# Kernel optimization log

Hardware: AMD Instinct MI355X
Metric: run time of the kernel (lower is better)

Reference implementation:

```python
import jax, jax.numpy as jnp
import numpy as np

B, C, N = 8, 512, 2048  # batch, channels (=size), tokens


def setup_inputs() -> dict:
    key = jax.random.key(0)
    ks = jax.random.split(key, 9)
    s = 1.0 / np.sqrt(C)
    return {
        "q": jax.random.normal(ks[0], (B, C, N), dtype=jnp.float32),
        "k": jax.random.normal(ks[1], (B, C, N), dtype=jnp.float32),
        "v": jax.random.normal(ks[2], (B, C, N), dtype=jnp.float32),
        "wq": jax.random.normal(ks[3], (C, C), dtype=jnp.float32) * s,
        "bq": jax.random.normal(ks[4], (C,), dtype=jnp.float32) * s,
        "wk": jax.random.normal(ks[5], (C, C), dtype=jnp.float32) * s,
        "bk": jax.random.normal(ks[6], (C,), dtype=jnp.float32) * s,
        "wv": jax.random.normal(ks[7], (C, C), dtype=jnp.float32) * s,
        "bv": jax.random.normal(ks[8], (C,), dtype=jnp.float32) * s,
    }


def _proj(x, w, b):
    # 1x1 conv over channels: out[b,c,n] = sum_i w[c,i] x[b,i,n] + b[c]
    return jnp.einsum('ci,bin->bcn', w, x) + b[None, :, None]


def reference(q, k, v, wq, bq, wk, bk, wv, bv):
    residual = q                                   # [B, C, N]
    qp = _proj(q, wq, bq).transpose(0, 2, 1)       # [B, N, C]
    kp = _proj(k, wk, bk).transpose(0, 2, 1)       # [B, N, C]
    vp = _proj(v, wv, bv).transpose(0, 2, 1)       # [B, N, C]
    attn = jnp.einsum('bnc,bmc->bnm', qp, kp)      # raw QK^T, no scale/softmax
    out = jnp.einsum('bnm,bmc->bnc', attn, vp)     # [B, N, C]
    return out.transpose(0, 2, 1) + residual       # [B, C, N]
```

## Files before the change

kernel.cpp:

```cpp
#include <hip/hip_runtime.h>
#include <hip/hip_bf16.h>
#include <stdint.h>

#define B_ 8
#define C_ 512
#define N_ 2048

typedef __bf16 bf16_t;
typedef bf16_t bf16x8 __attribute__((ext_vector_type(8)));
typedef bf16_t bf16x4 __attribute__((ext_vector_type(4)));
typedef float f32x4 __attribute__((ext_vector_type(4)));

__global__ __launch_bounds__(256) void prep_all_kernel(
    const float* __restrict__ q, const float* __restrict__ kin,
    const float* __restrict__ vin,
    const float* __restrict__ wq, const float* __restrict__ wk,
    const float* __restrict__ wv, const float* __restrict__ bq,
    const float* __restrict__ bk,
    bf16_t* __restrict__ qT, bf16_t* __restrict__ kc, bf16_t* __restrict__ vc,
    bf16_t* __restrict__ WqT, bf16_t* __restrict__ WkT, bf16_t* __restrict__ Wvb,
    float* __restrict__ s1p, float* __restrict__ sk, float* __restrict__ sv)
{
    __shared__ bf16_t tileA[64][65];
    __shared__ bf16_t tileB[64][65];
    __shared__ float red256[256];
    __shared__ float redr[4][4];
    const int bid = blockIdx.x;
    const int tid = threadIdx.x;

    if (bid < 1024) {
        const int b = bid >> 7;
        const int rem = bid & 127;
        const int c0 = (rem >> 4) * 64;
        const int n0 = (rem & 15) * 128;
        const float* src = q + (size_t)b * C_ * N_;
        bf16_t* dT = qT + (size_t)b * N_ * C_;
        const int cx = (tid & 15) * 4, ry = tid >> 4;
        float4 fa[4], fb[4];
#pragma unroll
        for (int p = 0; p < 4; ++p) {
            const int r = ry + p * 16;
            fa[p] = *(const float4*)&src[(size_t)(c0 + r) * N_ + n0 + cx];
            fb[p] = *(const float4*)&src[(size_t)(c0 + r) * N_ + n0 + 64 + cx];
        }
#pragma unroll
        for (int p = 0; p < 4; ++p) {
            const int r = ry + p * 16;
            tileA[r][cx + 0] = (bf16_t)fa[p].x; tileA[r][cx + 1] = (bf16_t)fa[p].y;
            tileA[r][cx + 2] = (bf16_t)fa[p].z; tileA[r][cx + 3] = (bf16_t)fa[p].w;
            tileB[r][cx + 0] = (bf16_t)fb[p].x; tileB[r][cx + 1] = (bf16_t)fb[p].y;
            tileB[r][cx + 2] = (bf16_t)fb[p].z; tileB[r][cx + 3] = (bf16_t)fb[p].w;
        }
        __syncthreads();
#pragma unroll
        for (int p = 0; p < 4; ++p) {
            const int r = ry + p * 16;
            bf16x4 o0, o1;
            o0[0] = tileA[cx + 0][r]; o0[1] = tileA[cx + 1][r];
            o0[2] = tileA[cx + 2][r]; o0[3] = tileA[cx + 3][r];
            *(bf16x4*)&dT[(size_t)(n0 + r) * C_ + c0 + cx] = o0;
            o1[0] = tileB[cx + 0][r]; o1[1] = tileB[cx + 1][r];
            o1[2] = tileB[cx + 2][r]; o1[3] = tileB[cx + 3][r];
            *(bf16x4*)&dT[(size_t)(n0 + 64 + r) * C_ + c0 + cx] = o1;
        }
    } else if (bid < 1217) {
        const int t = bid - 1024;
        if (t < 128) {
            const float* src = (t < 64) ? wq : wk;
            bf16_t* dst = (t < 64) ? WqT : WkT;
            const int j = t & 63;
            const int i0 = (j & 7) * 64, c0 = (j >> 3) * 64;
            const int cx = (tid & 15) * 4, ry = tid >> 4;
#pragma unroll
            for (int r = ry; r < 64; r += 16) {
                float4 f = *(const float4*)&src[(size_t)(c0 + r) * C_ + i0 + cx];
                tileA[r][cx + 0] = (bf16_t)f.x; tileA[r][cx + 1] = (bf16_t)f.y;
                tileA[r][cx + 2] = (bf16_t)f.z; tileA[r][cx + 3] = (bf16_t)f.w;
            }
            __syncthreads();
#pragma unroll
            for (int r = ry; r < 64; r += 16) {
                bf16x4 o;
                o[0] = tileA[cx + 0][r]; o[1] = tileA[cx + 1][r];
                o[2] = tileA[cx + 2][r]; o[3] = tileA[cx + 3][r];
                *(bf16x4*)&dst[(size_t)(i0 + r) * C_ + c0 + cx] = o;
            }
        } else if (t < 192) {
            const int j = t - 128;
#pragma unroll
            for (int p = 0; p < 4; ++p) {
                const int i = j * 4096 + p * 1024 + tid * 4;
                float4 f = *(const float4*)(wv + i);
                bf16x4 o;
                o[0] = (bf16_t)f.x; o[1] = (bf16_t)f.y;
                o[2] = (bf16_t)f.z; o[3] = (bf16_t)f.w;
                *(bf16x4*)(Wvb + i) = o;
            }
        } else {
            float p = bk[tid] * bq[tid] + bk[tid + 256] * bq[tid + 256];
            red256[tid] = p;
            __syncthreads();
            for (int s = 128; s > 0; s >>= 1) {
                if (tid < s) red256[tid] += red256[tid + s];
                __syncthreads();
            }
            if (tid == 0) s1p[0] = red256[0];
        }
    } else {
        const int r = bid - 1217;
        const int selv = r >> 10;
        const int row0 = (r & 1023) * 4;
        const float* src = (selv ? vin : kin) + (size_t)row0 * N_;
        bf16_t* dst = (selv ? vc : kc) + (size_t)row0 * N_;
        const int i = tid * 8;
        float4 f[4][2];
#pragma unroll
        for (int rr = 0; rr < 4; ++rr) {
            f[rr][0] = *(const float4*)(src + (size_t)rr * N_ + i);
            f[rr][1] = *(const float4*)(src + (size_t)rr * N_ + i + 4);
        }
        const int lane = tid & 63, wave = tid >> 6;
#pragma unroll
        for (int rr = 0; rr < 4; ++rr) {
            bf16x8 o;
            o[0] = (bf16_t)f[rr][0].x; o[1] = (bf16_t)f[rr][0].y;
            o[2] = (bf16_t)f[rr][0].z; o[3] = (bf16_t)f[rr][0].w;
            o[4] = (bf16_t)f[rr][1].x; o[5] = (bf16_t)f[rr][1].y;
            o[6] = (bf16_t)f[rr][1].z; o[7] = (bf16_t)f[rr][1].w;
            *(bf16x8*)(dst + (size_t)rr * N_ + i) = o;
            float s = f[rr][0].x + f[rr][0].y + f[rr][0].z + f[rr][0].w +
                      f[rr][1].x + f[rr][1].y + f[rr][1].z + f[rr][1].w;
#pragma unroll
            for (int d = 1; d < 64; d <<= 1) s += __shfl_xor(s, d, 64);
            if (lane == 0) redr[wave][rr] = s;
        }
        __syncthreads();
        if (tid < 4)
            (selv ? sv : sk)[row0 + tid] =
                redr[0][tid] + redr[1][tid] + redr[2][tid] + redr[3][tid];
    }
}

__global__ __launch_bounds__(256, 2) void dkv_M_kernel(
    const bf16_t* __restrict__ kc, const bf16_t* __restrict__ vc,
    bf16_t* __restrict__ Dp,
    const bf16_t* __restrict__ WqT, const bf16_t* __restrict__ WkT,
    bf16_t* __restrict__ M, const float* __restrict__ bq,
    const float* __restrict__ bk, float* __restrict__ gk,
    float* __restrict__ va)
{
    __shared__ __align__(16) bf16_t As[128 * 64];
    __shared__ __align__(16) bf16_t Bs[128 * 64];
    const int f = blockIdx.x;
    const int tid = threadIdx.x, lane = tid & 63, wave = tid >> 6;
    const int wr = wave >> 1, wc = wave & 1;
    const size_t sCC = (size_t)C_ * C_;
    const size_t sBN = (size_t)N_ * C_;

    if (f < 512) {
        const int zz = f >> 4;
        const int bz = zz >> 2, sp = zz & 3;
        const int t4 = f & 15;
        const int m0 = (t4 >> 2) * 128, n0 = (t4 & 3) * 128;
        const int kbeg = sp * 512;
        const bf16_t* Ab = kc + (size_t)bz * sBN;
        const bf16_t* Bb = vc + (size_t)bz * sBN;

        f32x4 acc[4][4];
#pragma unroll
        for (int i = 0; i < 4; ++i)
#pragma unroll
            for (int j = 0; j < 4; ++j) acc[i][j] = 0.f;

        const int srow = tid >> 3;
        const int scol = ((tid & 7) ^ (srow & 7)) * 8;
        const int ldso = tid * 16;

        for (int t = 0; t < 8; ++t) {
            const bf16_t* ga = Ab + (size_t)(m0 + srow) * N_ + kbeg + t * 64 + scol;
            const bf16_t* gb = Bb + (size_t)(n0 + srow) * N_ + kbeg + t * 64 + scol;
#pragma unroll
            for (int p = 0; p < 4; ++p)
                __builtin_amdgcn_global_load_lds(
                    (const __attribute__((address_space(1))) void*)(ga + (size_t)p * 32 * N_),
                    (__attribute__((address_space(3))) void*)((char*)As + ldso + p * 4096),
                    16, 0, 0);
#pragma unroll
            for (int p = 0; p < 4; ++p)
                __builtin_amdgcn_global_load_lds(
                    (const __attribute__((address_space(1))) void*)(gb + (size_t)p * 32 * N_),
                    (__attribute__((address_space(3))) void*)((char*)Bs + ldso + p * 4096),
                    16, 0, 0);
            __syncthreads();

#pragma unroll
            for (int kk = 0; kk < 64; kk += 32) {
                bf16x8 af[4], bfr[4];
                const int kcol = kk + (lane >> 4) * 8;
                const int kcn = kcol >> 3;
#pragma unroll
                for (int m = 0; m < 4; ++m) {
                    const int r = wr * 64 + (lane & 15) + m * 16;
                    af[m] = *(const bf16x8*)((const char*)As + r * 128 +
                                             ((kcn ^ (r & 7)) << 4));
                }
#pragma unroll
                for (int n = 0; n < 4; ++n) {
                    const int r = wc * 64 + (lane & 15) + n * 16;
                    bfr[n] = *(const bf16x8*)((const char*)Bs + r * 128 +
                                              ((kcn ^ (r & 7)) << 4));
                }
#pragma unroll
                for (int m = 0; m < 4; ++m)
#pragma unroll
                    for (int n = 0; n < 4; ++n)
                        acc[m][n] = __builtin_amdgcn_mfma_f32_16x16x32_bf16(
                            af[m], bfr[n], acc[m][n], 0, 0, 0);
            }
            __syncthreads();
        }

        const int rj = (lane >> 4) * 4;
        const int cc = lane & 15;
#pragma unroll
        for (int m = 0; m < 4; ++m)
#pragma unroll
            for (int n = 0; n < 4; ++n) {
                const int col = n0 + wc * 64 + n * 16 + cc;
                f32x4 vv = acc[m][n];
#pragma unroll
                for (int j = 0; j < 4; ++j) {
                    const int row = m0 + wr * 64 + m * 16 + rj + j;
                    Dp[(size_t)zz * sCC + (size_t)row * C_ + col] = (bf16_t)vv[j];
                }
            }
    } else if (f < 576) {
        const int g = f - 512;
        const int m0 = (g >> 3) * 64, n0 = (g & 7) * 64;
        f32x4 acc[2][2];
#pragma unroll
        for (int i = 0; i < 2; ++i)
#pragma unroll
            for (int j = 0; j < 2; ++j) acc[i][j] = 0.f;
        const int srow = tid >> 3;
        const int scol = ((tid & 7) ^ (srow & 7)) * 8;
        const int ldso = tid * 16;
        for (int t = 0; t < 8; ++t) {
            const bf16_t* ga = WqT + (size_t)(m0 + srow) * C_ + t * 64 + scol;
            const bf16_t* gb = WkT + (size_t)(n0 + srow) * C_ + t * 64 + scol;
#pragma unroll
            for (int p = 0; p < 2; ++p)
                __builtin_amdgcn_global_load_lds(
                    (const __attribute__((address_space(1))) void*)(ga + (size_t)p * 32 * C_),
                    (__attribute__((address_space(3))) void*)((char*)As + ldso + p * 4096),
                    16, 0, 0);
#pragma unroll
            for (int p = 0; p < 2; ++p)
                __builtin_amdgcn_global_load_lds(
                    (const __attribute__((address_space(1))) void*)(gb + (size_t)p * 32 * C_),
                    (__attribute__((address_space(3))) void*)((char*)Bs + ldso + p * 4096),
                    16, 0, 0);
            __syncthreads();
#pragma unroll
            for (int kk = 0; kk < 64; kk += 32) {
                bf16x8 af[2], bfr[2];
                const int kcol = kk + (lane >> 4) * 8;
                const int kcn = kcol >> 3;
#pragma unroll
                for (int m = 0; m < 2; ++m) {
                    const int r = wr * 32 + (lane & 15) + m * 16;
                    af[m] = *(const bf16x8*)((const char*)As + r * 128 +
                                             ((kcn ^ (r & 7)) << 4));
                }
#pragma unroll
                for (int n = 0; n < 2; ++n) {
                    const int r = wc * 32 + (lane & 15) + n * 16;
                    bfr[n] = *(const bf16x8*)((const char*)Bs + r * 128 +
                                              ((kcn ^ (r & 7)) << 4));
                }
#pragma unroll
                for (int m = 0; m < 2; ++m)
#pragma unroll
                    for (int n = 0; n < 2; ++n)
                        acc[m][n] = __builtin_amdgcn_mfma_f32_16x16x32_bf16(
                            af[m], bfr[n], acc[m][n], 0, 0, 0);
            }
            __syncthreads();
        }
        const int rj = (lane >> 4) * 4;
        const int cc = lane & 15;
#pragma unroll
        for (int m = 0; m < 2; ++m)
#pragma unroll
            for (int n = 0; n < 2; ++n) {
                const int col = n0 + wc * 32 + n * 16 + cc;
                f32x4 vv = acc[m][n];
#pragma unroll
                for (int j = 0; j < 4; ++j) {
                    const int row = m0 + wr * 32 + m * 16 + rj + j;
                    M[(size_t)row * C_ + col] = (bf16_t)vv[j];
                }
            }
    } else {
        const int j = f - 576;
        const bf16_t* W = (j < 8) ? WkT : WqT;
        const float* bb = (j < 8) ? bq : bk;
        float* out = (j < 8) ? gk : va;
        const int row = (j & 7) * 64 + (tid >> 2);
        const int c0 = (tid & 3) * 128;
        const bf16_t* rp = W + (size_t)row * C_ + c0;
        float acc = 0.f;
#pragma unroll
        for (int e = 0; e < 128; e += 8) {
            bf16x8 vv = *(const bf16x8*)(rp + e);
#pragma unroll
            for (int x = 0; x < 8; ++x) acc += (float)vv[x] * bb[c0 + e + x];
        }
        acc += __shfl_xor(acc, 1, 64);
        acc += __shfl_xor(acc, 2, 64);
        if ((tid & 3) == 0) out[row] = acc;
    }
}

__global__ __launch_bounds__(256) void p1_fused_kernel(
    const bf16_t* __restrict__ Wvb, const bf16_t* __restrict__ Dp,
    bf16_t* __restrict__ P1, const bf16_t* __restrict__ M,
    const float* __restrict__ sk, const float* __restrict__ sv,
    const float* __restrict__ gk, const float* __restrict__ s1p,
    float* __restrict__ u, float* __restrict__ vbraw, float* __restrict__ s2)
{
    __shared__ __align__(16) bf16_t As[64 * 64];
    __shared__ __align__(16) bf16_t Bs[64 * 64];
    __shared__ float svec[C_];
    __shared__ float red[256];
    const int f = blockIdx.x;
    const int tid = threadIdx.x, lane = tid & 63, wave = tid >> 6;
    const int wr = wave >> 1, wc = wave & 1;
    const size_t sCC = (size_t)C_ * C_;

    if (f < 512) {
        const int bz = f >> 6;
        const int m0 = ((f >> 3) & 7) * 64, n0 = (f & 7) * 64;
        f32x4 acc[2][2];
#pragma unroll
        for (int i = 0; i < 2; ++i)
#pragma unroll
            for (int j = 0; j < 2; ++j) acc[i][j] = 0.f;
        const int srow = tid >> 3;
        const int scol = ((tid & 7) ^ (srow & 7)) * 8;
        const int ldso = tid * 16;

        for (int sp = 0; sp < 4; ++sp) {
            const bf16_t* Bb = Dp + (size_t)(bz * 4 + sp) * sCC;
            for (int t = 0; t < 8; ++t) {
                const bf16_t* ga = Wvb + (size_t)(m0 + srow) * C_ + t * 64 + scol;
                const bf16_t* gb = Bb + (size_t)(n0 + srow) * C_ + t * 64 + scol;
#pragma unroll
                for (int p = 0; p < 2; ++p)
                    __builtin_amdgcn_global_load_lds(
                        (const __attribute__((address_space(1))) void*)(ga + (size_t)p * 32 * C_),
                        (__attribute__((address_space(3))) void*)((char*)As + ldso + p * 4096),
                        16, 0, 0);
#pragma unroll
                for (int p = 0; p < 2; ++p)
                    __builtin_amdgcn_global_load_lds(
                        (const __attribute__((address_space(1))) void*)(gb + (size_t)p * 32 * C_),
                        (__attribute__((address_space(3))) void*)((char*)Bs + ldso + p * 4096),
                        16, 0, 0);
                __syncthreads();
#pragma unroll
                for (int kk = 0; kk < 64; kk += 32) {
                    bf16x8 af[2], bfr[2];
                    const int kcol = kk + (lane >> 4) * 8;
                    const int kcn = kcol >> 3;
#pragma unroll
                    for (int m = 0; m < 2; ++m) {
                        const int r = wr * 32 + (lane & 15) + m * 16;
                        af[m] = *(const bf16x8*)((const char*)As + r * 128 +
                                                 ((kcn ^ (r & 7)) << 4));
                    }
#pragma unroll
                    for (int n = 0; n < 2; ++n) {
                        const int r = wc * 32 + (lane & 15) + n * 16;
                        bfr[n] = *(const bf16x8*)((const char*)Bs + r * 128 +
                                                  ((kcn ^ (r & 7)) << 4));
                    }
#pragma unroll
                    for (int m = 0; m < 2; ++m)
#pragma unroll
                        for (int n = 0; n < 2; ++n)
                            acc[m][n] = __builtin_amdgcn_mfma_f32_16x16x32_bf16(
                                af[m], bfr[n], acc[m][n], 0, 0, 0);
                }
                __syncthreads();
            }
        }
        const int rj = (lane >> 4) * 4;
        const int cc = lane & 15;
#pragma unroll
        for (int m = 0; m < 2; ++m)
#pragma unroll
            for (int n = 0; n < 2; ++n) {
                const int col = n0 + wc * 32 + n * 16 + cc;
                f32x4 vv = acc[m][n];
#pragma unroll
                for (int j = 0; j < 4; ++j) {
                    const int row = m0 + wr * 32 + m * 16 + rj + j;
                    P1[(size_t)bz * sCC + (size_t)row * C_ + col] = (bf16_t)vv[j];
                }
            }
    } else if (f < 520) {
        const int b = f - 512;
        const float* s4 = sv + (size_t)b * C_;
        svec[tid * 2] = s4[tid * 2];
        svec[tid * 2 + 1] = s4[tid * 2 + 1];
        __syncthreads();
        const int c = tid * 2;
#pragma unroll
        for (int rr = 0; rr < 2; ++rr) {
            const bf16_t* row = Wvb + (size_t)(c + rr) * C_;
            float acc = 0.f;
            for (int j = 0; j < C_; j += 8) {
                bf16x8 vv = *(const bf16x8*)(row + j);
#pragma unroll
                for (int e = 0; e < 8; ++e) acc += (float)vv[e] * svec[j + e];
            }
            u[b * C_ + c + rr] = acc;
        }
    } else {
        const int b = f - 520;
        const float* s4 = sk + (size_t)b * C_;
        svec[tid * 2] = s4[tid * 2];
        svec[tid * 2 + 1] = s4[tid * 2 + 1];
        __syncthreads();
        const int c = tid * 2;
#pragma unroll
        for (int rr = 0; rr < 2; ++rr) {
            const bf16_t* row = M + (size_t)(c + rr) * C_;
            float acc = 0.f;
            for (int j = 0; j < C_; j += 8) {
                bf16x8 vv = *(const bf16x8*)(row + j);
#pragma unroll
                for (int e = 0; e < 8; ++e) acc += (float)vv[e] * svec[j + e];
            }
            vbraw[b * C_ + c + rr] = acc;
        }
        float p = svec[tid] * gk[tid] + svec[tid + 256] * gk[tid + 256];
        red[tid] = p;
        __syncthreads();
        for (int s = 128; s > 0; s >>= 1) {
            if (tid < s) red[tid] += red[tid + s];
            __syncthreads();
        }
        if (tid == 0) s2[b] = red[0] + 2048.0f * s1p[0];
    }
}

__global__ __launch_bounds__(256) void gemm_ht(
    const bf16_t* __restrict__ A, const bf16_t* __restrict__ Bm,
    bf16_t* __restrict__ Cout,
    const float* __restrict__ e0, const float* __restrict__ e1,
    const float* __restrict__ e2, const float* __restrict__ e3,
    const float* __restrict__ bqv, float* __restrict__ hout,
    const float* __restrict__ s1p, const float* __restrict__ s2p)
{
    __shared__ __align__(16) bf16_t As[64 * 64];
    __shared__ __align__(16) bf16_t Bs[64 * 64];

    const int tid = threadIdx.x, lane = tid & 63, wave = tid >> 6;
    const int wr = wave >> 1, wc = wave & 1;
    const int bz = blockIdx.z;
    const int m0 = blockIdx.y * 64, n0 = blockIdx.x * 64;
    const size_t sCC = (size_t)C_ * C_;

    const bf16_t* Ab = A + (size_t)bz * sCC;

    f32x4 acc[2][2];
#pragma unroll
    for (int i = 0; i < 2; ++i)
#pragma unroll
        for (int j = 0; j < 2; ++j) acc[i][j] = 0.f;

    const int srow = tid >> 3;
    const int scol = ((tid & 7) ^ (srow & 7)) * 8;
    const int ldso = tid * 16;

    float hacc = 0.f;
    const bool doH = (blockIdx.x == 0);

    for (int t = 0; t < 8; ++t) {
        const bf16_t* ga = Ab + (size_t)(m0 + srow) * C_ + t * 64 + scol;
        const bf16_t* gb = Bm + (size_t)(n0 + srow) * C_ + t * 64 + scol;
#pragma unroll
        for (int p = 0; p < 2; ++p)
            __builtin_amdgcn_global_load_lds(
                (const __attribute__((address_space(1))) void*)(ga + (size_t)p * 32 * C_),
                (__attribute__((address_space(3))) void*)((char*)As + ldso + p * 4096),
                16, 0, 0);
#pragma unroll
        for (int p = 0; p < 2; ++p)
            __builtin_amdgcn_global_load_lds(
                (const __attribute__((address_space(1))) void*)(gb + (size_t)p * 32 * C_),
                (__attribute__((address_space(3))) void*)((char*)Bs + ldso + p * 4096),
                16, 0, 0);
        __syncthreads();

#pragma unroll
        for (int kk = 0; kk < 64; kk += 32) {
            bf16x8 af[2], bfr[2];
            const int kcol = kk + (lane >> 4) * 8;
            const int kcn = kcol >> 3;
#pragma unroll
            for (int m = 0; m < 2; ++m) {
                const int r = wr * 32 + (lane & 15) + m * 16;
                af[m] = *(const bf16x8*)((const char*)As + r * 128 +
                                         ((kcn ^ (r & 7)) << 4));
            }
#pragma unroll
            for (int n = 0; n < 2; ++n) {
                const int r = wc * 32 + (lane & 15) + n * 16;
                bfr[n] = *(const bf16x8*)((const char*)Bs + r * 128 +
                                          ((kcn ^ (r & 7)) << 4));
            }
#pragma unroll
            for (int m = 0; m < 2; ++m)
#pragma unroll
                for (int n = 0; n < 2; ++n)
                    acc[m][n] = __builtin_amdgcn_mfma_f32_16x16x32_bf16(
                        af[m], bfr[n], acc[m][n], 0, 0, 0);
        }
        if (doH) {
            const int rr = tid >> 2, qq = tid & 3;
#pragma unroll
            for (int uq = 0; uq < 2; ++uq) {
                const int c = qq * 2 + uq;
                bf16x8 av = *(const bf16x8*)((const char*)As + rr * 128 +
                                             ((c ^ (rr & 7)) << 4));
                const float* bp = bqv + t * 64 + c * 8;
#pragma unroll
                for (int e = 0; e < 8; ++e) hacc += (float)av[e] * bp[e];
            }
        }
        __syncthreads();
    }

    const int rj = (lane >> 4) * 4;
    const int cc = lane & 15;
#pragma unroll
    for (int m = 0; m < 2; ++m) {
#pragma unroll
        for (int n = 0; n < 2; ++n) {
            const int col = n0 + wc * 32 + n * 16 + cc;
            f32x4 vv = acc[m][n];
#pragma unroll
            for (int j = 0; j < 4; ++j) {
                const int row = m0 + wr * 32 + m * 16 + rj + j;
                float val = vv[j] + e0[bz * C_ + row] * e1[col] +
                            e2[row] * (e3[bz * C_ + col] + 2048.0f * e1[col]);
                Cout[(size_t)bz * sCC + (size_t)row * C_ + col] = (bf16_t)val;
            }
        }
    }
    if (doH) {
        hacc += __shfl_xor(hacc, 1, 64);
        hacc += __shfl_xor(hacc, 2, 64);
        if ((tid & 3) == 0) {
            const int row = m0 + (tid >> 2);
            hout[bz * C_ + row] = hacc + e0[bz * C_ + row] * s1p[0] +
                                  e2[row] * s2p[bz];
        }
    }
}

__global__ __launch_bounds__(256) void gemm_final(
    const bf16_t* __restrict__ A, const bf16_t* __restrict__ Bm,
    float* __restrict__ Cout, const float* __restrict__ qres,
    const float* __restrict__ hvec)
{
    __shared__ __align__(16) bf16_t As[128 * 64];
    __shared__ __align__(16) bf16_t Bs[128 * 64];

    const int f = blockIdx.x;
    const int xcd = f & 7, sl = f >> 3;
    const int g = xcd + 8 * (sl >> 2);
    const int m0 = (sl & 3) * 128;
    const int bz = g >> 4;
    const int n0 = (g & 15) * 128;
    const int K = C_;

    const int tid = threadIdx.x, lane = tid & 63, wave = tid >> 6;
    const int wr = wave >> 1, wc = wave & 1;

    const bf16_t* Ab = A + (size_t)bz * ((size_t)C_ * C_);
    const bf16_t* Bb = Bm + (size_t)bz * ((size_t)N_ * C_);

    f32x4 acc[4][4];
#pragma unroll
    for (int i = 0; i < 4; ++i)
#pragma unroll
        for (int j = 0; j < 4; ++j) acc[i][j] = 0.f;

    const int srow = tid >> 3;
    const int scol = ((tid & 7) ^ (srow & 7)) * 8;
    const int ldso = tid * 16;

    for (int t = 0; t < 8; ++t) {
        const bf16_t* ga = Ab + (size_t)(m0 + srow) * K + t * 64 + scol;
        const bf16_t* gb = Bb + (size_t)(n0 + srow) * K + t * 64 + scol;
#pragma unroll
        for (int p = 0; p < 4; ++p)
            __builtin_amdgcn_global_load_lds(
                (const __attribute__((address_space(1))) void*)(ga + (size_t)p * 32 * K),
                (__attribute__((address_space(3))) void*)((char*)As + ldso + p * 4096),
                16, 0, 0);
#pragma unroll
        for (int p = 0; p < 4; ++p)
            __builtin_amdgcn_global_load_lds(
                (const __attribute__((address_space(1))) void*)(gb + (size_t)p * 32 * K),
                (__attribute__((address_space(3))) void*)((char*)Bs + ldso + p * 4096),
                16, 0, 0);
        __syncthreads();

#pragma unroll
        for (int kk = 0; kk < 64; kk += 32) {
            bf16x8 af[4], bfr[4];
            const int kcol = kk + (lane >> 4) * 8;
            const int kcn = kcol >> 3;
#pragma unroll
            for (int m = 0; m < 4; ++m) {
                const int r = wr * 64 + (lane & 15) + m * 16;
                af[m] = *(const bf16x8*)((const char*)As + r * 128 +
                                         ((kcn ^ (r & 7)) << 4));
            }
#pragma unroll
            for (int n = 0; n < 4; ++n) {
                const int r = wc * 64 + (lane & 15) + n * 16;
                bfr[n] = *(const bf16x8*)((const char*)Bs + r * 128 +
                                          ((kcn ^ (r & 7)) << 4));
            }
#pragma unroll
            for (int m = 0; m < 4; ++m)
#pragma unroll
                for (int n = 0; n < 4; ++n)
                    acc[m][n] = __builtin_amdgcn_mfma_f32_16x16x32_bf16(
                        af[m], bfr[n], acc[m][n], 0, 0, 0);
        }
        __syncthreads();
    }

    const int rj = (lane >> 4) * 4;
    const int cc = lane & 15;
    const size_t ob = (size_t)bz * ((size_t)C_ * N_);
#pragma unroll
    for (int m = 0; m < 4; ++m) {
#pragma unroll
        for (int n = 0; n < 4; ++n) {
            const int col = n0 + wc * 64 + n * 16 + cc;
            f32x4 vv = acc[m][n];
#pragma unroll
            for (int j = 0; j < 4; ++j) {
                const int row = m0 + wr * 64 + m * 16 + rj + j;
                const size_t o = ob + (size_t)row * N_ + col;
                Cout[o] = vv[j] + hvec[bz * C_ + row] + qres[o];
            }
        }
    }
}

extern "C" void kernel_launch(void* const* d_in, const int* in_sizes, int n_in,
                              void* d_out, int out_size, void* d_ws, size_t ws_size,
                              hipStream_t stream)
{
    (void)in_sizes; (void)n_in; (void)out_size; (void)ws_size;
    const float* q  = (const float*)d_in[0];
    const float* k  = (const float*)d_in[1];
    const float* v  = (const float*)d_in[2];
    const float* wq = (const float*)d_in[3];
    const float* bq = (const float*)d_in[4];
    const float* wk = (const float*)d_in[5];
    const float* bk = (const float*)d_in[6];
    const float* wv = (const float*)d_in[7];
    const float* bv = (const float*)d_in[8];
    float* out = (float*)d_out;

    char* ws = (char*)d_ws;
    const size_t WSZ = (size_t)C_ * C_ * 2;
    const size_t TSZ = (size_t)B_ * N_ * C_ * 2;
    const size_t SCZ = (size_t)B_ * C_ * C_ * 2;
    const size_t VSZ = (size_t)B_ * C_ * 4;
    size_t off = 0;
    bf16_t* WqTb = (bf16_t*)(ws + off); off += WSZ;
    bf16_t* WkTb = (bf16_t*)(ws + off); off += WSZ;
    bf16_t* Wvb  = (bf16_t*)(ws + off); off += WSZ;
    bf16_t* M    = (bf16_t*)(ws + off); off += WSZ;
    bf16_t* qT   = (bf16_t*)(ws + off); off += TSZ;
    bf16_t* kc   = (bf16_t*)(ws + off); off += TSZ;
    bf16_t* vc   = (bf16_t*)(ws + off); off += TSZ;
    bf16_t* Dp   = (bf16_t*)(ws + off); off += TSZ;
    bf16_t* P1   = (bf16_t*)(ws + off); off += SCZ;
    bf16_t* HT   = (bf16_t*)(ws + off); off += SCZ;
    float*  sk   = (float*)(ws + off);  off += VSZ;
    float*  sv   = (float*)(ws + off);  off += VSZ;
    float*  gk   = (float*)(ws + off);  off += C_ * 4;
    float*  va   = (float*)(ws + off);  off += C_ * 4;
    float*  s1p  = (float*)(ws + off);  off += 64;
    float*  s2   = (float*)(ws + off);  off += 64;
    float*  uu   = (float*)(ws + off);  off += VSZ;
    float*  vbr  = (float*)(ws + off);  off += VSZ;
    float*  hb   = (float*)(ws + off);  off += VSZ;

    const dim3 blk(256);

    prep_all_kernel<<<dim3(3265), blk, 0, stream>>>(
        q, k, v, wq, wk, wv, bq, bk, qT, kc, vc, WqTb, WkTb, Wvb, s1p, sk, sv);

    dkv_M_kernel<<<dim3(592), blk, 0, stream>>>(
        kc, vc, Dp, WqTb, WkTb, M, bq, bk, gk, va);

    p1_fused_kernel<<<dim3(528), blk, 0, stream>>>(
        Wvb, Dp, P1, M, sk, sv, gk, s1p, uu, vbr, s2);

    gemm_ht<<<dim3(8, 8, B_), blk, 0, stream>>>(
        P1, M, HT, uu, va, bv, vbr, gk, hb, s1p, s2);

    gemm_final<<<dim3(512), blk, 0, stream>>>(HT, qT, out, q, hb);
}
```

Measured before the change: 111.6 us.

## Move q transpose-convert from prep kernel into the Dkv/M GEMM kernel

The q→bf16 transpose blocks are taken out of the prep kernel and added as 2048 extra 64x64 tile blocks in the second kernel, after the 512 Dkv GEMM blocks. The intent is to overlap this memory-bound transpose with the compute-bound GEMM work and shorten the prep kernel. The tile reuses the GEMM's shared-memory buffer, so occupancy stays at the GEMM's limit. The tiles are also smaller than before (64 columns instead of 128), so more blocks are launched.

Result: no change. 113.0 us (+1.2%).

```diff
diff --git a/kernel.cpp b/kernel.cpp
--- a/kernel.cpp
+++ b/kernel.cpp
@@ -11,103 +11,23 @@
 typedef bf16_t bf16x4 __attribute__((ext_vector_type(4)));
 typedef float f32x4 __attribute__((ext_vector_type(4)));
 
-__global__ __launch_bounds__(256) void prep_all_kernel(
-    const float* __restrict__ q, const float* __restrict__ kin,
-    const float* __restrict__ vin,
+__global__ __launch_bounds__(256) void prep_kernel(
+    const float* __restrict__ kin, const float* __restrict__ vin,
     const float* __restrict__ wq, const float* __restrict__ wk,
     const float* __restrict__ wv, const float* __restrict__ bq,
     const float* __restrict__ bk,
-    bf16_t* __restrict__ qT, bf16_t* __restrict__ kc, bf16_t* __restrict__ vc,
+    bf16_t* __restrict__ kc, bf16_t* __restrict__ vc,
     bf16_t* __restrict__ WqT, bf16_t* __restrict__ WkT, bf16_t* __restrict__ Wvb,
     float* __restrict__ s1p, float* __restrict__ sk, float* __restrict__ sv)
 {
     __shared__ bf16_t tileA[64][65];
-    __shared__ bf16_t tileB[64][65];
     __shared__ float red256[256];
     __shared__ float redr[4][4];
     const int bid = blockIdx.x;
     const int tid = threadIdx.x;
 
-    if (bid < 1024) {
-        const int b = bid >> 7;
-        const int rem = bid & 127;
-        const int c0 = (rem >> 4) * 64;
-        const int n0 = (rem & 15) * 128;
-        const float* src = q + (size_t)b * C_ * N_;
-        bf16_t* dT = qT + (size_t)b * N_ * C_;
-        const int cx = (tid & 15) * 4, ry = tid >> 4;
-        float4 fa[4], fb[4];
-#pragma unroll
-        for (int p = 0; p < 4; ++p) {
-            const int r = ry + p * 16;
-            fa[p] = *(const float4*)&src[(size_t)(c0 + r) * N_ + n0 + cx];
-            fb[p] = *(const float4*)&src[(size_t)(c0 + r) * N_ + n0 + 64 + cx];
-        }
-#pragma unroll
-        for (int p = 0; p < 4; ++p) {
-            const int r = ry + p * 16;
-            tileA[r][cx + 0] = (bf16_t)fa[p].x; tileA[r][cx + 1] = (bf16_t)fa[p].y;
-            tileA[r][cx + 2] = (bf16_t)fa[p].z; tileA[r][cx + 3] = (bf16_t)fa[p].w;
-            tileB[r][cx + 0] = (bf16_t)fb[p].x; tileB[r][cx + 1] = (bf16_t)fb[p].y;
-            tileB[r][cx + 2] = (bf16_t)fb[p].z; tileB[r][cx + 3] = (bf16_t)fb[p].w;
-        }
-        __syncthreads();
-#pragma unroll
-        for (int p = 0; p < 4; ++p) {
-            const int r = ry + p * 16;
-            bf16x4 o0, o1;
-            o0[0] = tileA[cx + 0][r]; o0[1] = tileA[cx + 1][r];
-            o0[2] = tileA[cx + 2][r]; o0[3] = tileA[cx + 3][r];
-            *(bf16x4*)&dT[(size_t)(n0 + r) * C_ + c0 + cx] = o0;
-            o1[0] = tileB[cx + 0][r]; o1[1] = tileB[cx + 1][r];
-            o1[2] = tileB[cx + 2][r]; o1[3] = tileB[cx + 3][r];
-            *(bf16x4*)&dT[(size_t)(n0 + 64 + r) * C_ + c0 + cx] = o1;
-        }
-    } else if (bid < 1217) {
-        const int t = bid - 1024;
-        if (t < 128) {
-            const float* src = (t < 64) ? wq : wk;
-            bf16_t* dst = (t < 64) ? WqT : WkT;
-            const int j = t & 63;
-            const int i0 = (j & 7) * 64, c0 = (j >> 3) * 64;
-            const int cx = (tid & 15) * 4, ry = tid >> 4;
-#pragma unroll
-            for (int r = ry; r < 64; r += 16) {
-                float4 f = *(const float4*)&src[(size_t)(c0 + r) * C_ + i0 + cx];
-                tileA[r][cx + 0] = (bf16_t)f.x; tileA[r][cx + 1] = (bf16_t)f.y;
-                tileA[r][cx + 2] = (bf16_t)f.z; tileA[r][cx + 3] = (bf16_t)f.w;
-            }
-            __syncthreads();
-#pragma unroll
-            for (int r = ry; r < 64; r += 16) {
-                bf16x4 o;
-                o[0] = tileA[cx + 0][r]; o[1] = tileA[cx + 1][r];
-                o[2] = tileA[cx + 2][r]; o[3] = tileA[cx + 3][r];
-                *(bf16x4*)&dst[(size_t)(i0 + r) * C_ + c0 + cx] = o;
-            }
-        } else if (t < 192) {
-            const int j = t - 128;
-#pragma unroll
-            for (int p = 0; p < 4; ++p) {
-                const int i = j * 4096 + p * 1024 + tid * 4;
-                float4 f = *(const float4*)(wv + i);
-                bf16x4 o;
-                o[0] = (bf16_t)f.x; o[1] = (bf16_t)f.y;
-                o[2] = (bf16_t)f.z; o[3] = (bf16_t)f.w;
-                *(bf16x4*)(Wvb + i) = o;
-            }
-        } else {
-            float p = bk[tid] * bq[tid] + bk[tid + 256] * bq[tid + 256];
-            red256[tid] = p;
-            __syncthreads();
-            for (int s = 128; s > 0; s >>= 1) {
-                if (tid < s) red256[tid] += red256[tid + s];
-                __syncthreads();
-            }
-            if (tid == 0) s1p[0] = red256[0];
-        }
-    } else {
-        const int r = bid - 1217;
+    if (bid < 2048) {
+        const int r = bid;
         const int selv = r >> 10;
         const int row0 = (r & 1023) * 4;
         const float* src = (selv ? vin : kin) + (size_t)row0 * N_;
@@ -138,12 +58,56 @@
         if (tid < 4)
             (selv ? sv : sk)[row0 + tid] =
                 redr[0][tid] + redr[1][tid] + redr[2][tid] + redr[3][tid];
+    } else {
+        const int t = bid - 2048;
+        if (t < 128) {
+            const float* src = (t < 64) ? wq : wk;
+            bf16_t* dst = (t < 64) ? WqT : WkT;
+            const int j = t & 63;
+            const int i0 = (j & 7) * 64, c0 = (j >> 3) * 64;
+            const int cx = (tid & 15) * 4, ry = tid >> 4;
+#pragma unroll
+            for (int r = ry; r < 64; r += 16) {
+                float4 f = *(const float4*)&src[(size_t)(c0 + r) * C_ + i0 + cx];
+                tileA[r][cx + 0] = (bf16_t)f.x; tileA[r][cx + 1] = (bf16_t)f.y;
+                tileA[r][cx + 2] = (bf16_t)f.z; tileA[r][cx + 3] = (bf16_t)f.w;
+            }
+            __syncthreads();
+#pragma unroll
+            for (int r = ry; r < 64; r += 16) {
+                bf16x4 o;
+                o[0] = tileA[cx + 0][r]; o[1] = tileA[cx + 1][r];
+                o[2] = tileA[cx + 2][r]; o[3] = tileA[cx + 3][r];
+                *(bf16x4*)&dst[(size_t)(i0 + r) * C_ + c0 + cx] = o;
+            }
+        } else if (t < 192) {
+            const int j = t - 128;
+#pragma unroll
+            for (int p = 0; p < 4; ++p) {
+                const int i = j * 4096 + p * 1024 + tid * 4;
+                float4 f = *(const float4*)(wv + i);
+                bf16x4 o;
+                o[0] = (bf16_t)f.x; o[1] = (bf16_t)f.y;
+                o[2] = (bf16_t)f.z; o[3] = (bf16_t)f.w;
+                *(bf16x4*)(Wvb + i) = o;
+            }
+        } else {
+            float p = bk[tid] * bq[tid] + bk[tid + 256] * bq[tid + 256];
+            red256[tid] = p;
+            __syncthreads();
+            for (int s = 128; s > 0; s >>= 1) {
+                if (tid < s) red256[tid] += red256[tid + s];
+                __syncthreads();
+            }
+            if (tid == 0) s1p[0] = red256[0];
+        }
     }
 }
 
-__global__ __launch_bounds__(256, 2) void dkv_M_kernel(
+__global__ __launch_bounds__(256, 2) void dkv_M_q_kernel(
     const bf16_t* __restrict__ kc, const bf16_t* __restrict__ vc,
-    bf16_t* __restrict__ Dp,
+    bf16_t* __restrict__ Dp, const float* __restrict__ q,
+    bf16_t* __restrict__ qT,
     const bf16_t* __restrict__ WqT, const bf16_t* __restrict__ WkT,
     bf16_t* __restrict__ M, const float* __restrict__ bq,
     const float* __restrict__ bk, float* __restrict__ gk,
@@ -234,8 +198,32 @@
                     Dp[(size_t)zz * sCC + (size_t)row * C_ + col] = (bf16_t)vv[j];
                 }
             }
-    } else if (f < 576) {
-        const int g = f - 512;
+    } else if (f < 2560) {
+        bf16_t (*tile)[65] = (bf16_t(*)[65])As;
+        const int t = f - 512;
+        const int b = t >> 8;
+        const int rem = t & 255;
+        const int c0 = (rem >> 5) * 64;
+        const int n0 = (rem & 31) * 64;
+        const float* src = q + (size_t)b * C_ * N_;
+        bf16_t* dT = qT + (size_t)b * N_ * C_;
+        const int cx = (tid & 15) * 4, ry = tid >> 4;
+#pragma unroll
+        for (int r = ry; r < 64; r += 16) {
+            float4 ff = *(const float4*)&src[(size_t)(c0 + r) * N_ + n0 + cx];
+            tile[r][cx + 0] = (bf16_t)ff.x; tile[r][cx + 1] = (bf16_t)ff.y;
+            tile[r][cx + 2] = (bf16_t)ff.z; tile[r][cx + 3] = (bf16_t)ff.w;
+        }
+        __syncthreads();
+#pragma unroll
+        for (int r = ry; r < 64; r += 16) {
+            bf16x4 o;
+            o[0] = tile[cx + 0][r]; o[1] = tile[cx + 1][r];
+            o[2] = tile[cx + 2][r]; o[3] = tile[cx + 3][r];
+            *(bf16x4*)&dT[(size_t)(n0 + r) * C_ + c0 + cx] = o;
+        }
+    } else if (f < 2624) {
+        const int g = f - 2560;
         const int m0 = (g >> 3) * 64, n0 = (g & 7) * 64;
         f32x4 acc[2][2];
 #pragma unroll
@@ -302,7 +290,7 @@
                 }
             }
     } else {
-        const int j = f - 576;
+        const int j = f - 2624;
         const bf16_t* W = (j < 8) ? WkT : WqT;
         const float* bb = (j < 8) ? bq : bk;
         float* out = (j < 8) ? gk : va;
@@ -711,11 +699,11 @@
 
     const dim3 blk(256);
 
-    prep_all_kernel<<<dim3(3265), blk, 0, stream>>>(
-        q, k, v, wq, wk, wv, bq, bk, qT, kc, vc, WqTb, WkTb, Wvb, s1p, sk, sv);
-
-    dkv_M_kernel<<<dim3(592), blk, 0, stream>>>(
-        kc, vc, Dp, WqTb, WkTb, M, bq, bk, gk, va);
+    prep_kernel<<<dim3(2241), blk, 0, stream>>>(
+        k, v, wq, wk, wv, bq, bk, kc, vc, WqTb, WkTb, Wvb, s1p, sk, sv);
+
+    dkv_M_q_kernel<<<dim3(2640), blk, 0, stream>>>(
+        kc, vc, Dp, q, qT, WqTb, WkTb, M, bq, bk, gk, va);
 
     p1_fused_kernel<<<dim3(528), blk, 0, stream>>>(
         Wvb, Dp, P1, M, sk, sv, gk, s1p, uu, vbr, s2);
```
